# Kernel tuning notes

Hardware: AMD Instinct MI355X
Metric: run time of the kernel (lower is better)

The kernel has to match this reference:

```python
import jax, jax.numpy as jnp
import numpy as np

B, CIN, COUT, H, W = 16, 512, 128, 64, 64


def setup_inputs() -> dict:
    key = jax.random.key(0)
    k1, k2, k3 = jax.random.split(key, 3)
    x = jax.random.normal(k1, (B, CIN, H, W), dtype=jnp.float32)
    style = jax.random.normal(k2, (B, CIN), dtype=jnp.float32)
    # kaiming_normal_ on [COUT, CIN, 1, 1]: fan_in = CIN*1*1, std = sqrt(2/fan_in)
    weight = jax.random.normal(k3, (COUT, CIN), dtype=jnp.float32) * np.float32(np.sqrt(2.0 / CIN))
    return {"x": x, "style": style, "weight": weight}


def reference(x, style, weight):
    # Per-sample modulated weight: mw[b,o,c] = style[b,c] * weight[o,c]
    # 1x1 conv, padding=0, stride=1 -> batched channel-mixing GEMM:
    # out[b,o,h,w] = sum_c mw[b,o,c] * x[b,c,h,w]
    return jnp.einsum('oc,bc,bchw->bohw', weight, style, x)
```

## Files before the change

kernel.cpp:

```cpp
#include <hip/hip_runtime.h>
#include <stdint.h>

#define NB    16
#define CIN   512
#define COUT  128
#define HW    4096
#define BN    64
#define BK    32
#define NIT   (CIN / BK)

using bf16x8  = __attribute__((ext_vector_type(8))) __bf16;
using floatx4 = __attribute__((ext_vector_type(4))) float;

__device__ __forceinline__ unsigned short f2bf_bits(float f) {
    union { float f; unsigned u; } v; v.f = f;
    return (unsigned short)((v.u + 0x7fffu + ((v.u >> 16) & 1u)) >> 16);
}

#define GLD16(g, l)                                                            \
    __builtin_amdgcn_global_load_lds(                                          \
        (const __attribute__((address_space(1))) void*)(g),                    \
        (__attribute__((address_space(3))) void*)(l), 16, 0, 0)

__global__ __launch_bounds__(256)
void modw_kernel(const float* __restrict__ style,
                 const float* __restrict__ weight,
                 __bf16* __restrict__ mw)
{
    const int id = blockIdx.x * 256 + threadIdx.x;
    const int k8 = id & 63;
    const int m  = (id >> 6) & 127;
    const int b  = id >> 13;

    const float4 w0 = *(const float4*)(weight + m * CIN + k8 * 8);
    const float4 w1 = *(const float4*)(weight + m * CIN + k8 * 8 + 4);
    const float4 s0 = *(const float4*)(style + b * CIN + k8 * 8);
    const float4 s1 = *(const float4*)(style + b * CIN + k8 * 8 + 4);

    union { unsigned short us[8]; bf16x8 v; } pk;
    pk.us[0] = f2bf_bits(w0.x * s0.x);
    pk.us[1] = f2bf_bits(w0.y * s0.y);
    pk.us[2] = f2bf_bits(w0.z * s0.z);
    pk.us[3] = f2bf_bits(w0.w * s0.w);
    pk.us[4] = f2bf_bits(w1.x * s1.x);
    pk.us[5] = f2bf_bits(w1.y * s1.y);
    pk.us[6] = f2bf_bits(w1.z * s1.z);
    pk.us[7] = f2bf_bits(w1.w * s1.w);
    *(bf16x8*)(mw + ((size_t)(b * 64 + k8) * 128 + m) * 8) = pk.v;
}

__global__ __launch_bounds__(256, 4)
void modconv1x1_kernel(const float* __restrict__ x,
                       const __bf16* __restrict__ mw,
                       float* __restrict__ out)
{
    __shared__ __align__(16) __bf16 Alds[2][4096];
    __shared__ __align__(16) float  Blds[2][BK * BN];

    const int tid  = threadIdx.x;
    const int lane = tid & 63;
    const int wave = tid >> 6;
    const int quad = lane >> 4;
    const int l15  = lane & 15;

    const int b  = blockIdx.x >> 6;
    const int n0 = (blockIdx.x & 63) * BN;

    const char*  xbb  = (const char*)(x + (size_t)b * CIN * HW + n0);
    float*       outb = out + (size_t)b * COUT * HW + n0;
    const char*  mwb  = (const char*)mw + (size_t)b * (64 * 128 * 16);

    const int wm = (wave & 1) * 64;
    const int wn = (wave >> 1) * 32;

    const int brow = lane >> 4;
    const int bcol = lane & 15;

    floatx4 acc[4][2];
    #pragma unroll
    for (int i = 0; i < 4; ++i)
        #pragma unroll
        for (int j = 0; j < 2; ++j)
            acc[i][j] = (floatx4){0.f, 0.f, 0.f, 0.f};

#define STAGE(K0, BUF)                                                         \
    {                                                                          \
        const char* at = mwb + (size_t)(K0) * 256;                             \
        char*       al = (char*)&Alds[BUF][0];                                 \
        GLD16(at + wave * 2048 + lane * 16,        al + wave * 2048);          \
        GLD16(at + wave * 2048 + 1024 + lane * 16, al + wave * 2048 + 1024);   \
        char* bl = (char*)&Blds[BUF][0];                                       \
        _Pragma("unroll")                                                      \
        for (int g = 0; g < 2; ++g) {                                          \
            const int r = wave * 8 + g * 4 + brow;                             \
            GLD16(xbb + (size_t)((K0) + r) * (HW * 4) + bcol * 16,             \
                  bl + (wave * 8 + g * 4) * 256);                              \
        }                                                                      \
    }

    STAGE(0, 0)

    int cur = 0;
    for (int it = 0; it < NIT; ++it) {
        __syncthreads();

        if (it + 1 < NIT) STAGE((it + 1) * BK, cur ^ 1)

        bf16x8 af[4];
        #pragma unroll
        for (int tm = 0; tm < 4; ++tm)
            af[tm] = *(const bf16x8*)&Alds[cur][(quad * COUT + wm + tm * 16 + l15) * 8];

        bf16x8 bfr[2];
        #pragma unroll
        for (int tn = 0; tn < 2; ++tn) {
            union { unsigned short us[8]; bf16x8 v; } pk;
            #pragma unroll
            for (int j = 0; j < 8; ++j)
                pk.us[j] = f2bf_bits(Blds[cur][(quad * 8 + j) * BN + wn + tn * 16 + l15]);
            bfr[tn] = pk.v;
        }

        #pragma unroll
        for (int tm = 0; tm < 4; ++tm)
            #pragma unroll
            for (int tn = 0; tn < 2; ++tn)
                acc[tm][tn] = __builtin_amdgcn_mfma_f32_16x16x32_bf16(
                    af[tm], bfr[tn], acc[tm][tn], 0, 0, 0);

        cur ^= 1;
    }
#undef STAGE

    #pragma unroll
    for (int tm = 0; tm < 4; ++tm) {
        const int o = wm + tm * 16 + quad * 4;
        #pragma unroll
        for (int tn = 0; tn < 2; ++tn) {
            const int n = wn + tn * 16 + l15;
            #pragma unroll
            for (int r = 0; r < 4; ++r)
                outb[(size_t)(o + r) * HW + n] = acc[tm][tn][r];
        }
    }
}

extern "C" void kernel_launch(void* const* d_in, const int* in_sizes, int n_in,
                              void* d_out, int out_size, void* d_ws, size_t ws_size,
                              hipStream_t stream) {
    const float* x      = (const float*)d_in[0];
    const float* style  = (const float*)d_in[1];
    const float* weight = (const float*)d_in[2];
    float* out = (float*)d_out;
    __bf16* mw = (__bf16*)d_ws;

    modw_kernel<<<dim3(512), dim3(256), 0, stream>>>(style, weight, mw);
    modconv1x1_kernel<<<dim3(NB * 64), dim3(256), 0, stream>>>(x, mw, out);
}
```

Measured before the change: 210.9 us.

## Load x tiles directly into registers and double waves per block

The B operand (x) is no longer staged through LDS with global_load_lds. Each lane now reads its eight fp32 values straight from global memory into registers and converts them to bf16 for the MFMA. Blocks grow to 512 threads (8 waves), and each wave covers a 16-column slice with a single N tile, so the LDS footprint and LDS read traffic shrink. The cost is that x loads are no longer prefetched a stage ahead: they are issued synchronously each iteration as 64-byte-wide strided row reads, which exposes global memory latency.

```diff
diff --git a/kernel.cpp b/kernel.cpp
--- a/kernel.cpp
+++ b/kernel.cpp
@@ -49,13 +49,12 @@
     *(bf16x8*)(mw + ((size_t)(b * 64 + k8) * 128 + m) * 8) = pk.v;
 }
 
-__global__ __launch_bounds__(256, 4)
+__global__ __launch_bounds__(512, 8)
 void modconv1x1_kernel(const float* __restrict__ x,
                        const __bf16* __restrict__ mw,
                        float* __restrict__ out)
 {
     __shared__ __align__(16) __bf16 Alds[2][4096];
-    __shared__ __align__(16) float  Blds[2][BK * BN];
 
     const int tid  = threadIdx.x;
     const int lane = tid & 63;
@@ -66,82 +65,65 @@
     const int b  = blockIdx.x >> 6;
     const int n0 = (blockIdx.x & 63) * BN;
 
-    const char*  xbb  = (const char*)(x + (size_t)b * CIN * HW + n0);
+    const int wm = (wave & 1) * 64;
+    const int wn = (wave >> 1) * 16;
+
+    const float* xbw  = x   + (size_t)b * CIN * HW + n0 + wn;
     float*       outb = out + (size_t)b * COUT * HW + n0;
     const char*  mwb  = (const char*)mw + (size_t)b * (64 * 128 * 16);
 
-    const int wm = (wave & 1) * 64;
-    const int wn = (wave >> 1) * 32;
+    floatx4 acc[4];
+    #pragma unroll
+    for (int i = 0; i < 4; ++i) acc[i] = (floatx4){0.f, 0.f, 0.f, 0.f};
 
-    const int brow = lane >> 4;
-    const int bcol = lane & 15;
-
-    floatx4 acc[4][2];
-    #pragma unroll
-    for (int i = 0; i < 4; ++i)
-        #pragma unroll
-        for (int j = 0; j < 2; ++j)
-            acc[i][j] = (floatx4){0.f, 0.f, 0.f, 0.f};
-
-#define STAGE(K0, BUF)                                                         \
-    {                                                                          \
-        const char* at = mwb + (size_t)(K0) * 256;                             \
-        char*       al = (char*)&Alds[BUF][0];                                 \
-        GLD16(at + wave * 2048 + lane * 16,        al + wave * 2048);          \
-        GLD16(at + wave * 2048 + 1024 + lane * 16, al + wave * 2048 + 1024);   \
-        char* bl = (char*)&Blds[BUF][0];                                       \
-        _Pragma("unroll")                                                      \
-        for (int g = 0; g < 2; ++g) {                                          \
-            const int r = wave * 8 + g * 4 + brow;                             \
-            GLD16(xbb + (size_t)((K0) + r) * (HW * 4) + bcol * 16,             \
-                  bl + (wave * 8 + g * 4) * 256);                              \
-        }                                                                      \
+    {
+        char* al = (char*)&Alds[0][0];
+        GLD16(mwb + wave * 1024 + lane * 16, al + wave * 1024);
     }
-
-    STAGE(0, 0)
 
     int cur = 0;
     for (int it = 0; it < NIT; ++it) {
+        const int k0 = it * BK;
         __syncthreads();
 
-        if (it + 1 < NIT) STAGE((it + 1) * BK, cur ^ 1)
+        if (it + 1 < NIT) {
+            const char* at = mwb + (size_t)(it + 1) * BK * 256;
+            char*       al = (char*)&Alds[cur ^ 1][0];
+            GLD16(at + wave * 1024 + lane * 16, al + wave * 1024);
+        }
+
+        float rbf[8];
+        {
+            const float* src = xbw + (size_t)(k0 + quad * 8) * HW + l15;
+            #pragma unroll
+            for (int j = 0; j < 8; ++j)
+                rbf[j] = src[(size_t)j * HW];
+        }
 
         bf16x8 af[4];
         #pragma unroll
         for (int tm = 0; tm < 4; ++tm)
             af[tm] = *(const bf16x8*)&Alds[cur][(quad * COUT + wm + tm * 16 + l15) * 8];
 
-        bf16x8 bfr[2];
+        union { unsigned short us[8]; bf16x8 v; } pk;
         #pragma unroll
-        for (int tn = 0; tn < 2; ++tn) {
-            union { unsigned short us[8]; bf16x8 v; } pk;
-            #pragma unroll
-            for (int j = 0; j < 8; ++j)
-                pk.us[j] = f2bf_bits(Blds[cur][(quad * 8 + j) * BN + wn + tn * 16 + l15]);
-            bfr[tn] = pk.v;
-        }
+        for (int j = 0; j < 8; ++j) pk.us[j] = f2bf_bits(rbf[j]);
 
         #pragma unroll
         for (int tm = 0; tm < 4; ++tm)
-            #pragma unroll
-            for (int tn = 0; tn < 2; ++tn)
-                acc[tm][tn] = __builtin_amdgcn_mfma_f32_16x16x32_bf16(
-                    af[tm], bfr[tn], acc[tm][tn], 0, 0, 0);
+            acc[tm] = __builtin_amdgcn_mfma_f32_16x16x32_bf16(
+                af[tm], pk.v, acc[tm], 0, 0, 0);
 
         cur ^= 1;
     }
-#undef STAGE
 
     #pragma unroll
     for (int tm = 0; tm < 4; ++tm) {
         const int o = wm + tm * 16 + quad * 4;
+        const int n = wn + l15;
         #pragma unroll
-        for (int tn = 0; tn < 2; ++tn) {
-            const int n = wn + tn * 16 + l15;
-            #pragma unroll
-            for (int r = 0; r < 4; ++r)
-                outb[(size_t)(o + r) * HW + n] = acc[tm][tn][r];
-        }
+        for (int r = 0; r < 4; ++r)
+            outb[(size_t)(o + r) * HW + n] = acc[tm][r];
     }
 }
 
@@ -155,5 +137,5 @@
     __bf16* mw = (__bf16*)d_ws;
 
     modw_kernel<<<dim3(512), dim3(256), 0, stream>>>(style, weight, mw);
-    modconv1x1_kernel<<<dim3(NB * 64), dim3(256), 0, stream>>>(x, mw, out);
+    modconv1x1_kernel<<<dim3(NB * BN), dim3(512), 0, stream>>>(x, mw, out);
 }
```

Result: no change. 212.9 us (+0.9%).
